# Performance work log

Measured on AMD Instinct MI355X. Metric: run time of the kernel, lower is better.

The kernel has to match this reference:

```python
import jax, jax.numpy as jnp
import numpy as np


def pairwise_distance(x):
    # x: [B,N,F] -> squared euclidean distance matrix [B,N,N]
    sq = jnp.sum(x * x, axis=-1)
    d = sq[:, :, None] + sq[:, None, :] - 2.0 * jnp.einsum('bnd,bmd->bnm', x, x)
    return jnp.maximum(d, 0.0)


def knn_adjacency(dist, k):
    # keep the k nearest neighbors of each point (binary adjacency)
    B, N, _ = dist.shape
    idx = jax.lax.top_k(-dist, k)[1]  # [B,N,k]
    A = jnp.zeros((B, N, N), dist.dtype)
    return A.at[jnp.arange(B)[:, None, None], jnp.arange(N)[None, :, None], idx].set(1.0)


def get_laplacian(A):
    # normalized graph Laplacian L = I - D^{-1/2} A D^{-1/2}
    d = jnp.sum(A, axis=-1)
    dinv = jnp.where(d > 0, 1.0 / jnp.sqrt(jnp.maximum(d, 1e-12)), 0.0)
    An = A * dinv[:, :, None] * dinv[:, None, :]
    return jnp.eye(A.shape[-1], dtype=A.dtype)[None] - An


def cheb_conv(x, L, W, b, K):
    # DenseChebConv: Chebyshev recurrence T0=x, T1=Lx, Tk=2L T_{k-1}-T_{k-2};
    # concat along features then dense projection. x:[B,N,Fin], W:[K*Fin,Fout]
    xs = [x]
    if K > 1:
        xs.append(jnp.einsum('bnm,bmf->bnf', L, x))
    for _ in range(2, K):
        xs.append(2.0 * jnp.einsum('bnm,bmf->bnf', L, xs[-1]) - xs[-2])
    xk = jnp.concatenate(xs, axis=-1)
    return jnp.einsum('bnf,fo->bno', xk, W) + b


def segment_max(out, idx):
    # fused replacement of the per-batch/per-cluster python loops:
    # out:[B,N,F], idx:[B,R,S] -> max-pooled cluster features [B,R,F]
    B = out.shape[0]
    g = out[jnp.arange(B)[:, None, None], idx]  # [B,R,S,F]
    return jnp.max(g, axis=2)


def setup_inputs():
    key = jax.random.key(0)
    ks = jax.random.split(key, 12)
    B, N, R, S, P = 32, 1024, 64, 16, 55
    inp = {}
    inp['x'] = jax.random.normal(ks[0], (B, N, 7), jnp.float32)
    inp['x2'] = jax.random.normal(ks[1], (B, N, 3), jnp.float32)
    inp['laplacian_Reeb'] = jax.random.normal(ks[2], (B, R, R), jnp.float32)
    inp['W1'] = jax.random.normal(ks[3], (3 * 7, 64), jnp.float32) * 0.1
    inp['b1'] = jnp.zeros((64,), jnp.float32)
    inp['W_reeb'] = jax.random.normal(ks[4], (6 * 64, 256), jnp.float32) * 0.05
    inp['b_reeb'] = jnp.zeros((256,), jnp.float32)
    inp['W_fps'] = jax.random.normal(ks[5], (6 * 64, 256), jnp.float32) * 0.05
    inp['b_fps'] = jnp.zeros((256,), jnp.float32)
    inp['fc1_w'] = jax.random.normal(ks[6], (512, 256), jnp.float32) * 0.05
    inp['fc1_b'] = jnp.zeros((256,), jnp.float32)
    inp['fc3_w'] = jax.random.normal(ks[7], (256, 40), jnp.float32) * 0.05
    inp['fc3_b'] = jnp.zeros((40,), jnp.float32)
    inp['sccs'] = jax.random.randint(ks[8], (B, R, S), 0, N)
    inp['sccs_fps'] = jax.random.randint(ks[9], (B, P, N), 0, N)
    inp['k'] = 30
    inp['batch_size'] = B
    inp['num_points'] = N
    return inp


def reference(x, x2, laplacian_Reeb, W1, b1, W_reeb, b_reeb, W_fps, b_fps,
              fc1_w, fc1_b, fc3_w, fc3_b, sccs, sccs_fps, k, batch_size, num_points):
    sg = jax.lax.stop_gradient
    # point-cloud kNN Laplacian (torch.no_grad in original)
    L = sg(get_laplacian(knn_adjacency(pairwise_distance(x), k)))
    out = jax.nn.relu(cheb_conv(x, L, W1, b1, 3))  # [B,N,64]
    reg1 = jnp.sum(jnp.einsum('bnf,bnm,bmg->bfg', out, L, out) ** 2)
    # Reeb-graph segment max pooling (no_grad in original)
    V_reeb = sg(segment_max(out, sccs))  # [B,R,64]
    L_reeb = sg(laplacian_Reeb)
    out_reeb = jax.nn.relu(cheb_conv(V_reeb, L_reeb, W_reeb, b_reeb, 6))  # [B,R,256]
    reg2 = jnp.sum(jnp.einsum('bnf,bnm,bmg->bfg', out_reeb, L_reeb, out_reeb) ** 2)
    # FPS cluster max pooling (no_grad in original)
    V_fps = sg(segment_max(out, sccs_fps))  # [B,55,64]
    L_fps = sg(get_laplacian(pairwise_distance(V_fps)))
    out_fps = jax.nn.relu(cheb_conv(V_fps, L_fps, W_fps, b_fps, 6))  # [B,55,256]
    reg3 = jnp.sum(jnp.einsum('bnf,bnm,bmg->bfg', out_fps, L_fps, out_fps) ** 2)
    feat = jnp.concatenate([jnp.max(out_reeb, axis=1), jnp.max(out_fps, axis=1)], axis=1)  # [B,512]
    h = jax.nn.relu(feat @ fc1_w + fc1_b)
    logits = h @ fc3_w + fc3_b  # [B,40]
    regs = jnp.stack([reg1, reg2, reg3,
                      jnp.sum(fc1_w[:, 0] ** 2), fc1_b[0] ** 2,
                      jnp.sum(fc3_w[:, 0] ** 2), fc3_b[0] ** 2])
    return logits, regs
```

## Files before the change

### kernel.cpp

```cpp
#include <hip/hip_runtime.h>
#include <math.h>

#define BN 32
#define NP 1024
#define KNN 30
#define NR 64
#define NFPS 55

#define XSLOT(r) ((r) * 8 + ((r) >> 7) * 4)

__device__ __forceinline__ float lap_s() {
    const float dv = 1.0f / sqrtf(30.0f);
    return dv * dv;
}

__device__ __forceinline__ float dist7(const float4& xiA, const float4& xiB,
                                       float sqi, const float4& ca, const float4& cb) {
#pragma clang fp contract(off)
    float dot = xiA.x * ca.x;
    dot = fmaf(xiA.y, ca.y, dot);
    dot = fmaf(xiA.z, ca.z, dot);
    dot = fmaf(xiA.w, ca.w, dot);
    dot = fmaf(xiB.x, cb.x, dot);
    dot = fmaf(xiB.y, cb.y, dot);
    dot = fmaf(xiB.z, cb.z, dot);
    float r = sqi + cb.w;
    r = r - 2.f * dot;
    return fmaxf(r, 0.f);
}

__global__ __launch_bounds__(256, 4) void k_knn(const float* __restrict__ x,
                                                int* __restrict__ knn,
                                                float* __restrict__ xs1) {
    __shared__ float xls[8224];
    int b = blockIdx.x;
    int t = threadIdx.x;
    int ln = t & 63, wv = t >> 6;
    int seg = ln & 7;
    int rl  = ln >> 3;

    const float* xb = x + (size_t)b * NP * 7;
#pragma unroll 4
    for (int k = 0; k < 32; ++k) {
        int q = k * 256 + t;
        int r = q >> 3, d = q & 7;
        float v = (d < 7) ? xb[r * 7 + d] : 0.f;
        float p2 = v * v;
        p2 += __shfl_xor(p2, 1);
        p2 += __shfl_xor(p2, 2);
        p2 += __shfl_xor(p2, 4);
        xls[XSLOT(r) + d] = (d < 7) ? v : p2;
    }
    __syncthreads();

    int grow = blockIdx.y * 32 + wv * 8 + rl;
    int gslot = XSLOT(grow);
    float4 xiA = *(const float4*)&xls[gslot];
    float4 xiB = *(const float4*)&xls[gslot + 4];
    float sqi = xiB.w;

    float bd[KNN];
#pragma unroll
    for (int q = 0; q < KNN; ++q) bd[q] = __builtin_inff();
    int jbase = seg * 128;
    int sbase = XSLOT(jbase);
    for (int jc = 0; jc < 128; jc += 4) {
        const float* p = &xls[sbase + jc * 8];
        float4 a0 = *(const float4*)(p +  0), b0 = *(const float4*)(p +  4);
        float4 a1 = *(const float4*)(p +  8), b1 = *(const float4*)(p + 12);
        float4 a2 = *(const float4*)(p + 16), b2 = *(const float4*)(p + 20);
        float4 a3 = *(const float4*)(p + 24), b3 = *(const float4*)(p + 28);
        float d0 = dist7(xiA, xiB, sqi, a0, b0);
        float d1 = dist7(xiA, xiB, sqi, a1, b1);
        float d2 = dist7(xiA, xiB, sqi, a2, b2);
        float d3 = dist7(xiA, xiB, sqi, a3, b3);
#pragma unroll
        for (int q = KNN - 1; q >= 1; --q) bd[q] = __builtin_amdgcn_fmed3f(bd[q - 1], d0, bd[q]);
        bd[0] = fminf(bd[0], d0);
#pragma unroll
        for (int q = KNN - 1; q >= 1; --q) bd[q] = __builtin_amdgcn_fmed3f(bd[q - 1], d1, bd[q]);
        bd[0] = fminf(bd[0], d1);
#pragma unroll
        for (int q = KNN - 1; q >= 1; --q) bd[q] = __builtin_amdgcn_fmed3f(bd[q - 1], d2, bd[q]);
        bd[0] = fminf(bd[0], d2);
#pragma unroll
        for (int q = KNN - 1; q >= 1; --q) bd[q] = __builtin_amdgcn_fmed3f(bd[q - 1], d3, bd[q]);
        bd[0] = fminf(bd[0], d3);
    }

    float m[32];
#pragma unroll
    for (int q = 0; q < KNN; ++q) m[q] = bd[q];
    m[30] = __builtin_inff(); m[31] = __builtin_inff();
#pragma unroll
    for (int lvl = 0; lvl < 3; ++lvl) {
        int mask = 1 << lvl;
#pragma unroll
        for (int q = 0; q < 16; ++q) {
            float u = __shfl_xor(m[31 - q], mask);
            float v = __shfl_xor(m[q], mask);
            float lo = fminf(m[q], u);
            float hi = fminf(m[31 - q], v);
            m[q] = lo; m[31 - q] = hi;
        }
#pragma unroll
        for (int d = 16; d >= 1; d >>= 1) {
#pragma unroll
            for (int i = 0; i < 32; ++i) {
                if ((i & d) == 0) {
                    float a = m[i], c = m[i | d];
                    m[i] = fminf(a, c);
                    m[i | d] = fmaxf(a, c);
                }
            }
        }
    }
    float T = m[29];
    int firstT = 0;
#pragma unroll
    for (int q = 0; q < KNN; ++q) firstT += (m[q] < T) ? 1 : 0;
    int need = KNN - firstT;
    int cnt_lt = 0, cnt_eq = 0;
#pragma unroll
    for (int q = 0; q < KNN; ++q) {
        cnt_lt += (bd[q] < T) ? 1 : 0;
        cnt_eq += (bd[q] == T) ? 1 : 0;
    }
    int lanebase = ln & ~7;
    int pe = 0;
#pragma unroll
    for (int s2 = 0; s2 < 7; ++s2) {
        int v = __shfl(cnt_eq, lanebase + s2);
        pe += (s2 < seg) ? v : 0;
    }
    int e = need - pe;
    e = (e < 0) ? 0 : e;
    e = (e > cnt_eq) ? cnt_eq : e;
    int tk = cnt_lt + e;
    int pb = 0;
#pragma unroll
    for (int s2 = 0; s2 < 7; ++s2) {
        int v = __shfl(tk, lanebase + s2);
        pb += (s2 < seg) ? v : 0;
    }
    int base = pb;

    int* kout = knn + ((size_t)b * NP + grow) * KNN;
    float n0 = 0.f, n1 = 0.f, n2 = 0.f, n3 = 0.f, n4 = 0.f, n5 = 0.f, n6 = 0.f;
    int cs = 0, ct = 0;
    for (int jc = 0; jc < 128; jc += 4) {
        const float* p = &xls[sbase + jc * 8];
        float4 a0 = *(const float4*)(p +  0), b0 = *(const float4*)(p +  4);
        float4 a1 = *(const float4*)(p +  8), b1 = *(const float4*)(p + 12);
        float4 a2 = *(const float4*)(p + 16), b2 = *(const float4*)(p + 20);
        float4 a3 = *(const float4*)(p + 24), b3 = *(const float4*)(p + 28);
        float d0 = dist7(xiA, xiB, sqi, a0, b0);
        float d1 = dist7(xiA, xiB, sqi, a1, b1);
        float d2 = dist7(xiA, xiB, sqi, a2, b2);
        float d3 = dist7(xiA, xiB, sqi, a3, b3);
#pragma unroll
        for (int u = 0; u < 4; ++u) {
            float dist = (u == 0) ? d0 : (u == 1) ? d1 : (u == 2) ? d2 : d3;
            const float4& ca = (u == 0) ? a0 : (u == 1) ? a1 : (u == 2) ? a2 : a3;
            const float4& cb = (u == 0) ? b0 : (u == 1) ? b1 : (u == 2) ? b2 : b3;
            bool lt = dist < T;
            bool eq = (dist == T) && (ct < e);
            if ((lt || eq) && (cs + ct < tk)) {
                kout[base + cs + ct] = jbase + jc + u;
                cs += lt ? 1 : 0;
                ct += eq ? 1 : 0;
                n0 += ca.x; n1 += ca.y; n2 += ca.z; n3 += ca.w;
                n4 += cb.x; n5 += cb.y; n6 += cb.z;
            }
        }
    }
#pragma unroll
    for (int mask = 1; mask <= 4; mask <<= 1) {
        n0 += __shfl_xor(n0, mask);
        n1 += __shfl_xor(n1, mask);
        n2 += __shfl_xor(n2, mask);
        n3 += __shfl_xor(n3, mask);
        n4 += __shfl_xor(n4, mask);
        n5 += __shfl_xor(n5, mask);
        n6 += __shfl_xor(n6, mask);
    }
    if (seg < 7) {
        float nv = (seg == 0) ? n0 : (seg == 1) ? n1 : (seg == 2) ? n2 :
                   (seg == 3) ? n3 : (seg == 4) ? n4 : (seg == 5) ? n5 : n6;
        xs1[((size_t)b * NP + grow) * 7 + seg] = xls[gslot + seg] - lap_s() * nv;
    }
}

__global__ __launch_bounds__(256) void k_out(const float* __restrict__ x,
                                             const float* __restrict__ xs1,
                                             const int* __restrict__ knn,
                                             const float* __restrict__ W1,
                                             const float* __restrict__ b1,
                                             float* __restrict__ out,
                                             const float* __restrict__ fc1_w,
                                             const float* __restrict__ fc1_b,
                                             const float* __restrict__ fc3_w,
                                             const float* __restrict__ fc3_b,
                                             float* __restrict__ regs,
                                             float* __restrict__ Cbuf) {
    __shared__ float x1s[NP * 7];
    __shared__ float x0s[64 * 7];
    __shared__ float fr[64 * 21];
    __shared__ float W1s[21 * 64];
    __shared__ float b1s[64];
    int b = blockIdx.x, y = blockIdx.y;
    int t = threadIdx.x;
    if (y == 16) {
        float* cb = Cbuf + (size_t)b * 4096;
        for (int q = t; q < 4096; q += 256) cb[q] = 0.f;
        if (b != 0) return;
        float* r1 = x1s;
        float* r2 = x1s + 256;
        float s1 = 0.f;
        for (int i = t; i < 512; i += 256) { float v = fc1_w[(size_t)i * 256]; s1 += v * v; }
        float v2 = fc3_w[(size_t)t * 40];
        r1[t] = s1; r2[t] = v2 * v2;
        __syncthreads();
        for (int st = 128; st > 0; st >>= 1) {
            if (t < st) { r1[t] += r1[t + st]; r2[t] += r2[t + st]; }
            __syncthreads();
        }
        if (t == 0) {
            regs[0] = 0.f; regs[1] = 0.f; regs[2] = 0.f;
            regs[3] = r1[0];
            regs[4] = fc1_b[0] * fc1_b[0];
            regs[5] = r2[0];
            regs[6] = fc3_b[0] * fc3_b[0];
        }
        return;
    }
    int rbase = y * 64;
    for (int q = t; q < NP * 7; q += 256) x1s[q] = xs1[(size_t)b * NP * 7 + q];
    for (int q = t; q < 64 * 7; q += 256) x0s[q] = x[(size_t)b * NP * 7 + (size_t)rbase * 7 + q];
    for (int q = t; q < 21 * 64; q += 256) W1s[q] = W1[q];
    if (t < 64) b1s[t] = b1[t];
    __syncthreads();
    if (t < 64) {
        int i = rbase + t;
        float f[21];
#pragma unroll
        for (int d = 0; d < 7; ++d) { f[d] = x0s[t * 7 + d]; f[7 + d] = x1s[i * 7 + d]; }
        float ns[7] = {0.f, 0.f, 0.f, 0.f, 0.f, 0.f, 0.f};
        const int* kn = knn + ((size_t)b * NP + i) * KNN;
        for (int q = 0; q < KNN; ++q) {
            int j = kn[q];
#pragma unroll
            for (int d = 0; d < 7; ++d) ns[d] += x1s[j * 7 + d];
        }
        const float s = lap_s();
#pragma unroll
        for (int d = 0; d < 7; ++d) f[14 + d] = 2.f * (f[7 + d] - s * ns[d]) - f[d];
#pragma unroll
        for (int d = 0; d < 21; ++d) fr[t * 21 + d] = f[d];
    }
    __syncthreads();
    int o = t & 63, g = t >> 6;
    for (int m = 0; m < 16; ++m) {
        int r = g * 16 + m;
        float acc = b1s[o];
#pragma unroll
        for (int d = 0; d < 21; ++d) acc += fr[r * 21 + d] * W1s[d * 64 + o];
        out[((size_t)b * NP + rbase + r) * 64 + o] = fmaxf(acc, 0.f);
    }
}

__global__ __launch_bounds__(256) void k_z1v(const float* __restrict__ out,
                                             const int* __restrict__ knn,
                                             const int* __restrict__ sccs,
                                             const int* __restrict__ sccs_fps,
                                             float* __restrict__ Z1,
                                             float* __restrict__ Vr,
                                             float* __restrict__ Vf) {
    __shared__ unsigned bmw[32];
    __shared__ float red[256];
    int b = blockIdx.x, y = blockIdx.y;
    int t = threadIdx.x;
    const float* ob = out + (size_t)b * NP * 64;
    if (y < 256) {
        int i = y * 4 + (t >> 6);
        int f = t & 63;
        const int* kn = knn + ((size_t)b * NP + i) * KNN;
        float sum = 0.f;
        for (int q = 0; q < KNN; ++q) sum += ob[(size_t)kn[q] * 64 + f];
        Z1[((size_t)b * NP + i) * 64 + f] = ob[(size_t)i * 64 + f] - lap_s() * sum;
    } else if (y < 272) {
        int r = (y - 256) * 4 + (t >> 6);
        int f = t & 63;
        const int* sc = sccs + ((size_t)b * NR + r) * 16;
        float m = -__builtin_inff();
        for (int q = 0; q < 16; ++q) m = fmaxf(m, ob[(size_t)sc[q] * 64 + f]);
        Vr[((size_t)b * NR + r) * 64 + f] = m;
    } else {
        int p = y - 272;
        const int* sp = sccs_fps + ((size_t)b * NFPS + p) * 1024;
        if (t < 32) bmw[t] = 0u;
        __syncthreads();
        for (int q = t; q < 1024; q += 256) {
            int r = sp[q];
            atomicOr(&bmw[r >> 5], 1u << (r & 31));
        }
        __syncthreads();
        int f = t & 63, sc = t >> 6;
        float m = -__builtin_inff();
        for (int w0 = sc * 8; w0 < sc * 8 + 8; ++w0) {
            unsigned w = bmw[w0];
            while (w) {
                int bit = __ffs(w) - 1;
                w &= w - 1;
                m = fmaxf(m, ob[(size_t)(w0 * 32 + bit) * 64 + f]);
            }
        }
        red[t] = m; __syncthreads();
        if (sc == 0) {
            m = fmaxf(fmaxf(red[f], red[64 + f]), fmaxf(red[128 + f], red[192 + f]));
            Vf[((size_t)b * NFPS + p) * 64 + f] = m;
        }
    }
}

__device__ __forceinline__ void t1_part(const float* __restrict__ out,
                                        const float* __restrict__ Z1,
                                        float* __restrict__ Cbuf,
                                        float* buf, int y) {
    int b = blockIdx.x, t = threadIdx.x;
    float* os = buf;
    float* zs = buf + 8192;
    const float* ob = out + ((size_t)b * NP + (size_t)y * 128) * 64;
    const float* zb = Z1 + ((size_t)b * NP + (size_t)y * 128) * 64;
    for (int q = t; q < 128 * 64; q += 256) { os[q] = ob[q]; zs[q] = zb[q]; }
    __syncthreads();
    int f0 = (t & 15) * 4, g0 = (t >> 4) * 4;
    float4 ac0 = make_float4(0.f, 0.f, 0.f, 0.f);
    float4 ac1 = ac0, ac2 = ac0, ac3 = ac0;
#pragma unroll 4
    for (int n = 0; n < 128; ++n) {
        float4 ov = *(const float4*)&os[n * 64 + f0];
        float4 zv = *(const float4*)&zs[n * 64 + g0];
        ac0.x += ov.x * zv.x; ac0.y += ov.x * zv.y; ac0.z += ov.x * zv.z; ac0.w += ov.x * zv.w;
        ac1.x += ov.y * zv.x; ac1.y += ov.y * zv.y; ac1.z += ov.y * zv.z; ac1.w += ov.y * zv.w;
        ac2.x += ov.z * zv.x; ac2.y += ov.z * zv.y; ac2.z += ov.z * zv.z; ac2.w += ov.z * zv.w;
        ac3.x += ov.w * zv.x; ac3.y += ov.w * zv.y; ac3.z += ov.w * zv.z; ac3.w += ov.w * zv.w;
    }
    float* cb = Cbuf + (size_t)b * 4096;
    atomicAdd(&cb[(f0 + 0) * 64 + g0 + 0], ac0.x);
    atomicAdd(&cb[(f0 + 0) * 64 + g0 + 1], ac0.y);
    atomicAdd(&cb[(f0 + 0) * 64 + g0 + 2], ac0.z);
    atomicAdd(&cb[(f0 + 0) * 64 + g0 + 3], ac0.w);
    atomicAdd(&cb[(f0 + 1) * 64 + g0 + 0], ac1.x);
    atomicAdd(&cb[(f0 + 1) * 64 + g0 + 1], ac1.y);
    atomicAdd(&cb[(f0 + 1) * 64 + g0 + 2], ac1.z);
    atomicAdd(&cb[(f0 + 1) * 64 + g0 + 3], ac1.w);
    atomicAdd(&cb[(f0 + 2) * 64 + g0 + 0], ac2.x);
    atomicAdd(&cb[(f0 + 2) * 64 + g0 + 1], ac2.y);
    atomicAdd(&cb[(f0 + 2) * 64 + g0 + 2], ac2.z);
    atomicAdd(&cb[(f0 + 2) * 64 + g0 + 3], ac2.w);
    atomicAdd(&cb[(f0 + 3) * 64 + g0 + 0], ac3.x);
    atomicAdd(&cb[(f0 + 3) * 64 + g0 + 1], ac3.y);
    atomicAdd(&cb[(f0 + 3) * 64 + g0 + 2], ac3.z);
    atomicAdd(&cb[(f0 + 3) * 64 + g0 + 3], ac3.w);
}

__device__ __forceinline__ void lfps_impl(const float* __restrict__ Vfps,
                                          float* __restrict__ Lf, float* buf) {
    int b = blockIdx.x;
    int t = threadIdx.x;
    float* Vs = buf;
    float* sq = buf + 3520;
    float* dist = buf + 3584;
    float* dinv = buf + 6609;
    for (int q = t; q < NFPS * 64; q += 256) Vs[q] = Vfps[(size_t)b * NFPS * 64 + q];
    __syncthreads();
    if (t < NFPS) {
        float s = 0.f;
        for (int f = 0; f < 64; ++f) { float v = Vs[t * 64 + f]; s += v * v; }
        sq[t] = s;
    }
    __syncthreads();
    for (int q = t; q < NFPS * NFPS; q += 256) {
        int i = q / NFPS, j = q % NFPS;
        float dot = 0.f;
        for (int f = 0; f < 64; ++f) dot += Vs[i * 64 + f] * Vs[j * 64 + f];
        dist[q] = fmaxf(sq[i] + sq[j] - 2.f * dot, 0.f);
    }
    __syncthreads();
    if (t < NFPS) {
        float s = 0.f;
        for (int j = 0; j < NFPS; ++j) s += dist[t * NFPS + j];
        dinv[t] = (s > 0.f) ? 1.0f / sqrtf(fmaxf(s, 1e-12f)) : 0.f;
    }
    __syncthreads();
    for (int q = t; q < NFPS * NFPS; q += 256) {
        int i = q / NFPS, j = q % NFPS;
        Lf[(size_t)b * NFPS * NFPS + q] = ((i == j) ? 1.f : 0.f) - dist[q] * dinv[i] * dinv[j];
    }
}

template<int N>
__device__ __forceinline__ void cheb_impl(const float* __restrict__ L,
                                          const float* __restrict__ V,
                                          const float* __restrict__ W,
                                          const float* __restrict__ bias,
                                          float* __restrict__ out,
                                          float* __restrict__ Z,
                                          float* Ls, float* bA, float* bB, float* Ws,
                                          int b, int sl) {
    constexpr int NPAD = (N + 3) & ~3;
    int t = threadIdx.x;
    int c0 = (t & 15) * 4;
    int r0 = (t >> 4) * 4;

    for (int q = t; q < 64 * 64; q += 256) { Ls[q] = 0.f; bA[q] = 0.f; bB[q] = 0.f; }
    __syncthreads();
    for (int q = t; q < N * N; q += 256) {
        int r = q / N, m = q % N;
        Ls[r * 64 + m] = L[(size_t)b * N * N + q];
    }
    for (int q = t; q < N * 64; q += 256) bA[q] = V[(size_t)b * N * 64 + q];
    {
        const float* Wk = W + sl * 64;
        for (int q = t; q < 64 * 64; q += 256) Ws[q] = Wk[(q >> 6) * 256 + (q & 63)];
    }
    float4 a4[4];
    {
        float4 bv = *(const float4*)&bias[sl * 64 + c0];
#pragma unroll
        for (int i = 0; i < 4; ++i) a4[i] = bv;
    }
    __syncthreads();

    auto accum = [&](const float* xb) {
#pragma unroll 2
        for (int m = 0; m < 64; m += 4) {
            float4 xv[4], wv[4];
#pragma unroll
            for (int i = 0; i < 4; ++i) xv[i] = *(const float4*)&xb[(r0 + i) * 64 + m];
#pragma unroll
            for (int mm = 0; mm < 4; ++mm) wv[mm] = *(const float4*)&Ws[(m + mm) * 64 + c0];
#pragma unroll
            for (int i = 0; i < 4; ++i) {
                float xi0 = xv[i].x, xi1 = xv[i].y, xi2 = xv[i].z, xi3 = xv[i].w;
                a4[i].x += xi0 * wv[0].x; a4[i].y += xi0 * wv[0].y; a4[i].z += xi0 * wv[0].z; a4[i].w += xi0 * wv[0].w;
                a4[i].x += xi1 * wv[1].x; a4[i].y += xi1 * wv[1].y; a4[i].z += xi1 * wv[1].z; a4[i].w += xi1 * wv[1].w;
                a4[i].x += xi2 * wv[2].x; a4[i].y += xi2 * wv[2].y; a4[i].z += xi2 * wv[2].z; a4[i].w += xi2 * wv[2].w;
                a4[i].x += xi3 * wv[3].x; a4[i].y += xi3 * wv[3].y; a4[i].z += xi3 * wv[3].z; a4[i].w += xi3 * wv[3].w;
            }
        }
    };
    auto chebmm = [&](const float* src, float* dst, bool first) {
        float4 acc[4];
#pragma unroll
        for (int i = 0; i < 4; ++i) acc[i] = make_float4(0.f, 0.f, 0.f, 0.f);
#pragma unroll 2
        for (int m = 0; m < NPAD; m += 4) {
            float4 sv[4], lv[4];
#pragma unroll
            for (int mm = 0; mm < 4; ++mm) sv[mm] = *(const float4*)&src[(m + mm) * 64 + c0];
#pragma unroll
            for (int i = 0; i < 4; ++i) lv[i] = *(const float4*)&Ls[(r0 + i) * 64 + m];
#pragma unroll
            for (int i = 0; i < 4; ++i) {
                float l0 = lv[i].x, l1 = lv[i].y, l2 = lv[i].z, l3 = lv[i].w;
                acc[i].x += l0 * sv[0].x; acc[i].y += l0 * sv[0].y; acc[i].z += l0 * sv[0].z; acc[i].w += l0 * sv[0].w;
                acc[i].x += l1 * sv[1].x; acc[i].y += l1 * sv[1].y; acc[i].z += l1 * sv[1].z; acc[i].w += l1 * sv[1].w;
                acc[i].x += l2 * sv[2].x; acc[i].y += l2 * sv[2].y; acc[i].z += l2 * sv[2].z; acc[i].w += l2 * sv[2].w;
                acc[i].x += l3 * sv[3].x; acc[i].y += l3 * sv[3].y; acc[i].z += l3 * sv[3].z; acc[i].w += l3 * sv[3].w;
            }
        }
#pragma unroll
        for (int i = 0; i < 4; ++i) {
            if (r0 + i < N) {
                float4* d = (float4*)&dst[(r0 + i) * 64 + c0];
                if (first) *d = acc[i];
                else {
                    float4 od = *d;
                    *d = make_float4(2.f * acc[i].x - od.x, 2.f * acc[i].y - od.y,
                                     2.f * acc[i].z - od.z, 2.f * acc[i].w - od.w);
                }
            }
        }
    };
    auto loadW = [&](int k) {
        const float* Wk = W + (size_t)k * 64 * 256 + sl * 64;
        for (int q = t; q < 64 * 64; q += 256) Ws[q] = Wk[(q >> 6) * 256 + (q & 63)];
    };

    accum(bA);                 __syncthreads();
    chebmm(bA, bB, true);      loadW(1);  __syncthreads();
    accum(bB);                 __syncthreads();
    chebmm(bB, bA, false);     loadW(2);  __syncthreads();
    accum(bA);                 __syncthreads();
    chebmm(bA, bB, false);     loadW(3);  __syncthreads();
    accum(bB);                 __syncthreads();
    chebmm(bB, bA, false);     loadW(4);  __syncthreads();
    accum(bA);                 __syncthreads();
    chebmm(bA, bB, false);     loadW(5);  __syncthreads();
    accum(bB);                 __syncthreads();

    float* ob = out + (size_t)b * N * 256 + sl * 64;
#pragma unroll
    for (int i = 0; i < 4; ++i) {
        if (r0 + i < N) {
            float4 v = make_float4(fmaxf(a4[i].x, 0.f), fmaxf(a4[i].y, 0.f),
                                   fmaxf(a4[i].z, 0.f), fmaxf(a4[i].w, 0.f));
            *(float4*)&bA[(r0 + i) * 64 + c0] = v;
            *(float4*)&ob[(size_t)(r0 + i) * 256 + c0] = v;
        }
    }
    __syncthreads();
    {
        float4 acc[4];
#pragma unroll
        for (int i = 0; i < 4; ++i) acc[i] = make_float4(0.f, 0.f, 0.f, 0.f);
#pragma unroll 2
        for (int m = 0; m < NPAD; m += 4) {
            float4 sv[4], lv[4];
#pragma unroll
            for (int mm = 0; mm < 4; ++mm) sv[mm] = *(const float4*)&bA[(m + mm) * 64 + c0];
#pragma unroll
            for (int i = 0; i < 4; ++i) lv[i] = *(const float4*)&Ls[(r0 + i) * 64 + m];
#pragma unroll
            for (int i = 0; i < 4; ++i) {
                float l0 = lv[i].x, l1 = lv[i].y, l2 = lv[i].z, l3 = lv[i].w;
                acc[i].x += l0 * sv[0].x; acc[i].y += l0 * sv[0].y; acc[i].z += l0 * sv[0].z; acc[i].w += l0 * sv[0].w;
                acc[i].x += l1 * sv[1].x; acc[i].y += l1 * sv[1].y; acc[i].z += l1 * sv[1].z; acc[i].w += l1 * sv[1].w;
                acc[i].x += l2 * sv[2].x; acc[i].y += l2 * sv[2].y; acc[i].z += l2 * sv[2].z; acc[i].w += l2 * sv[2].w;
                acc[i].x += l3 * sv[3].x; acc[i].y += l3 * sv[3].y; acc[i].z += l3 * sv[3].z; acc[i].w += l3 * sv[3].w;
            }
        }
        float* zb = Z + (size_t)b * N * 256 + sl * 64;
#pragma unroll
        for (int i = 0; i < 4; ++i)
            if (r0 + i < N) *(float4*)&zb[(size_t)(r0 + i) * 256 + c0] = acc[i];
    }
}

template<int N>
__device__ __forceinline__ void treg_impl(const float* __restrict__ out,
                                          const float* __restrict__ Z,
                                          float* __restrict__ reg,
                                          float* zs, float* os, float* red, int y) {
    int b = blockIdx.x;
    int f0 = (y >> 1) * 32;
    int g0 = (y & 1) * 128;
    int t = threadIdx.x;
    for (int q = t; q < N * 128; q += 256) {
        int r = q >> 7, gl = q & 127;
        zs[q] = Z[(size_t)b * N * 256 + r * 256 + g0 + gl];
    }
    for (int q = t; q < N * 32; q += 256) {
        int r = q >> 5, f = q & 31;
        os[q] = out[(size_t)b * N * 256 + r * 256 + f0 + f];
    }
    __syncthreads();
    int fl = t >> 3;
    int gb = (t & 7) * 16;
    float accv[16];
#pragma unroll
    for (int q = 0; q < 16; ++q) accv[q] = 0.f;
    for (int n = 0; n < N; ++n) {
        float a = os[n * 32 + fl];
        const float* zr = zs + n * 128 + gb;
#pragma unroll
        for (int q = 0; q < 16; ++q) accv[q] += a * zr[q];
    }
    float loc = 0.f;
#pragma unroll
    for (int q = 0; q < 16; ++q) loc += accv[q] * accv[q];
    red[t] = loc; __syncthreads();
    for (int st = 128; st > 0; st >>= 1) { if (t < st) red[t] += red[t + st]; __syncthreads(); }
    if (t == 0) atomicAdd(reg, red[0]);
}

__global__ __launch_bounds__(256) void k_mid1(
        const float* __restrict__ out, const float* __restrict__ Z1,
        const float* __restrict__ Vfps, float* __restrict__ Cbuf,
        float* __restrict__ Lf,
        const float* __restrict__ Lr, const float* __restrict__ Vr,
        const float* __restrict__ Wr, const float* __restrict__ br,
        float* __restrict__ outR, float* __restrict__ Zr) {
    __shared__ float smem[16384];
    int y = blockIdx.y;
    if (y < 8)       t1_part(out, Z1, Cbuf, smem, y);
    else if (y == 8) lfps_impl(Vfps, Lf, smem);
    else cheb_impl<NR>(Lr, Vr, Wr, br, outR, Zr,
                       smem, smem + 4096, smem + 8192, smem + 12288,
                       blockIdx.x, y - 9);
}

__global__ __launch_bounds__(256) void k_mid2(
        const float* __restrict__ Lf, const float* __restrict__ Vf,
        const float* __restrict__ Wf, const float* __restrict__ bf,
        float* __restrict__ outP, float* __restrict__ Zf,
        const float* __restrict__ outR, const float* __restrict__ Zr,
        const float* __restrict__ Cbuf, float* __restrict__ regs) {
    __shared__ float smem[16384];
    int y = blockIdx.y;
    if (y < 4) cheb_impl<NFPS>(Lf, Vf, Wf, bf, outP, Zf,
                               smem, smem + 4096, smem + 8192, smem + 12288,
                               blockIdx.x, y);
    else if (y < 20) treg_impl<NR>(outR, Zr, regs + 1, smem, smem + 8192, smem + 10240, y - 4);
    else {
        int b = blockIdx.x, t = threadIdx.x;
        float* red = smem;
        float loc = 0.f;
        for (int q = t; q < 4096; q += 256) { float v = Cbuf[(size_t)b * 4096 + q]; loc += v * v; }
        red[t] = loc; __syncthreads();
        for (int st = 128; st > 0; st >>= 1) { if (t < st) red[t] += red[t + st]; __syncthreads(); }
        if (t == 0) atomicAdd(&regs[0], red[0]);
    }
}

__global__ __launch_bounds__(256) void k_fin(
        const float* __restrict__ outP, const float* __restrict__ Zf,
        const float* __restrict__ outR,
        const float* __restrict__ fc1_w, const float* __restrict__ fc1_b,
        const float* __restrict__ fc3_w, const float* __restrict__ fc3_b,
        float* __restrict__ regs, float* __restrict__ logits) {
    __shared__ float smem[10496];
    int y = blockIdx.y;
    if (y < 16) treg_impl<NFPS>(outP, Zf, regs + 2, smem, smem + 8192, smem + 10240, y);
    else {
        int b = blockIdx.x, t = threadIdx.x;
        float* feat = smem;
        float* h = smem + 8192;
        float m = -__builtin_inff();
        for (int r = 0; r < NR; ++r) m = fmaxf(m, outR[((size_t)b * NR + r) * 256 + t]);
        feat[t] = m;
        m = -__builtin_inff();
        for (int p = 0; p < NFPS; ++p) m = fmaxf(m, outP[((size_t)b * NFPS + p) * 256 + t]);
        feat[256 + t] = m;
        __syncthreads();
        float a = fc1_b[t];
        for (int i = 0; i < 512; ++i) a += feat[i] * fc1_w[(size_t)i * 256 + t];
        h[t] = fmaxf(a, 0.f);
        __syncthreads();
        if (t < 40) {
            float a2 = fc3_b[t];
            for (int i = 0; i < 256; ++i) a2 += h[i] * fc3_w[(size_t)i * 40 + t];
            logits[(size_t)b * 40 + t] = a2;
        }
    }
}

extern "C" void kernel_launch(void* const* d_in, const int* in_sizes, int n_in,
                              void* d_out, int out_size, void* d_ws, size_t ws_size,
                              hipStream_t stream) {
    const float* x      = (const float*)d_in[0];
    const float* L_reeb = (const float*)d_in[2];
    const float* W1     = (const float*)d_in[3];
    const float* b1     = (const float*)d_in[4];
    const float* W_reeb = (const float*)d_in[5];
    const float* b_reeb = (const float*)d_in[6];
    const float* W_fps  = (const float*)d_in[7];
    const float* b_fps  = (const float*)d_in[8];
    const float* fc1_w  = (const float*)d_in[9];
    const float* fc1_b  = (const float*)d_in[10];
    const float* fc3_w  = (const float*)d_in[11];
    const float* fc3_b  = (const float*)d_in[12];
    const int*   sccs   = (const int*)d_in[13];
    const int*   sccs_f = (const int*)d_in[14];

    float* outv = (float*)d_out;
    float* regs = outv + 1280;

    char* w = (char*)d_ws;
    size_t off = 0;
    auto alloc = [&](size_t bytes) { void* p = w + off; off = (off + bytes + 255) & ~(size_t)255; return p; };
    int*   knn   = (int*)  alloc((size_t)BN * NP * KNN * 4);
    float* xs1   = (float*)alloc((size_t)BN * NP * 7 * 4);
    float* outF  = (float*)alloc((size_t)BN * NP * 64 * 4);
    float* Z1    = (float*)alloc((size_t)BN * NP * 64 * 4);
    float* Vreeb = (float*)alloc((size_t)BN * NR * 64 * 4);
    float* outRb = (float*)alloc((size_t)BN * NR * 256 * 4);
    float* Z2    = (float*)alloc((size_t)BN * NR * 256 * 4);
    float* Vfps  = (float*)alloc((size_t)BN * NFPS * 64 * 4);
    float* Lfps  = (float*)alloc((size_t)BN * NFPS * NFPS * 4);
    float* outP  = (float*)alloc((size_t)BN * NFPS * 256 * 4);
    float* Z3    = (float*)alloc((size_t)BN * NFPS * 256 * 4);
    float* Cbuf  = (float*)alloc((size_t)BN * 4096 * 4);

    k_knn<<<dim3(BN, NP / 32), 256, 0, stream>>>(x, knn, xs1);
    k_out<<<dim3(BN, 17), 256, 0, stream>>>(x, xs1, knn, W1, b1, outF,
                                            fc1_w, fc1_b, fc3_w, fc3_b, regs, Cbuf);
    k_z1v<<<dim3(BN, 256 + 16 + NFPS), 256, 0, stream>>>(outF, knn, sccs, sccs_f,
                                                         Z1, Vreeb, Vfps);
    k_mid1<<<dim3(BN, 13), 256, 0, stream>>>(outF, Z1, Vfps, Cbuf, Lfps,
                                             L_reeb, Vreeb, W_reeb, b_reeb, outRb, Z2);
    k_mid2<<<dim3(BN, 21), 256, 0, stream>>>(Lfps, Vfps, W_fps, b_fps, outP, Z3,
                                             outRb, Z2, Cbuf, regs);
    k_fin<<<dim3(BN, 17), 256, 0, stream>>>(outP, Z3, outRb,
                                            fc1_w, fc1_b, fc3_w, fc3_b, regs, outv);
}
```

Measured before the change: 357.8 us.

## Compute full Chebyshev output per block, split kNN neighbor sums, pad kNN output

The Chebyshev conv kernels now compute all 256 output columns in one block per batch instead of splitting across four 64-column slices. This removes the redundant Chebyshev recurrence that each slice recomputed, at the cost of larger shared memory (112KB) and fewer, longer blocks. The k_out neighbor-sum gather is spread over four threads per row via a shared partial buffer instead of 64 threads. kNN output gains a fallback fill for unfilled slots.

After: 492.0 us. 37.5% more time.

```diff
diff --git a/kernel.cpp b/kernel.cpp
--- a/kernel.cpp
+++ b/kernel.cpp
@@ -12,6 +12,10 @@
 __device__ __forceinline__ float lap_s() {
     const float dv = 1.0f / sqrtf(30.0f);
     return dv * dv;
+}
+
+__device__ __forceinline__ float4 relu4(float4 v) {
+    return make_float4(fmaxf(v.x, 0.f), fmaxf(v.y, 0.f), fmaxf(v.z, 0.f), fmaxf(v.w, 0.f));
 }
 
 __device__ __forceinline__ float dist7(const float4& xiA, const float4& xiB,
@@ -174,6 +178,7 @@
             }
         }
     }
+    for (int q = cs + ct; q < tk; ++q) kout[base + q] = grow;
 #pragma unroll
     for (int mask = 1; mask <= 4; mask <<= 1) {
         n0 += __shfl_xor(n0, mask);
@@ -208,6 +213,7 @@
     __shared__ float fr[64 * 21];
     __shared__ float W1s[21 * 64];
     __shared__ float b1s[64];
+    __shared__ float nsp[64 * 28];
     int b = blockIdx.x, y = blockIdx.y;
     int t = threadIdx.x;
     if (y == 16) {
@@ -240,21 +246,32 @@
     for (int q = t; q < 21 * 64; q += 256) W1s[q] = W1[q];
     if (t < 64) b1s[t] = b1[t];
     __syncthreads();
+    {
+        int row = t >> 2, tq = t & 3;
+        int i = rbase + row;
+        float ns[7] = {0.f, 0.f, 0.f, 0.f, 0.f, 0.f, 0.f};
+        const int* kn = knn + ((size_t)b * NP + i) * KNN;
+        for (int q = tq; q < KNN; q += 4) {
+            int j = kn[q];
+#pragma unroll
+            for (int d = 0; d < 7; ++d) ns[d] += x1s[j * 7 + d];
+        }
+#pragma unroll
+        for (int d = 0; d < 7; ++d) nsp[row * 28 + tq * 7 + d] = ns[d];
+    }
+    __syncthreads();
     if (t < 64) {
         int i = rbase + t;
         float f[21];
 #pragma unroll
         for (int d = 0; d < 7; ++d) { f[d] = x0s[t * 7 + d]; f[7 + d] = x1s[i * 7 + d]; }
-        float ns[7] = {0.f, 0.f, 0.f, 0.f, 0.f, 0.f, 0.f};
-        const int* kn = knn + ((size_t)b * NP + i) * KNN;
-        for (int q = 0; q < KNN; ++q) {
-            int j = kn[q];
-#pragma unroll
-            for (int d = 0; d < 7; ++d) ns[d] += x1s[j * 7 + d];
-        }
         const float s = lap_s();
 #pragma unroll
-        for (int d = 0; d < 7; ++d) f[14 + d] = 2.f * (f[7 + d] - s * ns[d]) - f[d];
+        for (int d = 0; d < 7; ++d) {
+            float ns = nsp[t * 28 + d] + nsp[t * 28 + 7 + d]
+                     + nsp[t * 28 + 14 + d] + nsp[t * 28 + 21 + d];
+            f[14 + d] = 2.f * (f[7 + d] - s * ns) - f[d];
+        }
 #pragma unroll
         for (int d = 0; d < 21; ++d) fr[t * 21 + d] = f[d];
     }
@@ -401,53 +418,61 @@
 }
 
 template<int N>
-__device__ __forceinline__ void cheb_impl(const float* __restrict__ L,
+__device__ __forceinline__ void cheb_full(const float* __restrict__ L,
                                           const float* __restrict__ V,
                                           const float* __restrict__ W,
                                           const float* __restrict__ bias,
                                           float* __restrict__ out,
                                           float* __restrict__ Z,
-                                          float* Ls, float* bA, float* bB, float* Ws,
-                                          int b, int sl) {
+                                          float* smem, int b) {
     constexpr int NPAD = (N + 3) & ~3;
+    float* Ls = smem;
+    float* bA = smem + 4096;
+    float* bB = smem + 8192;
+    float* Ws = smem + 12288;
     int t = threadIdx.x;
-    int c0 = (t & 15) * 4;
-    int r0 = (t >> 4) * 4;
+    int c0 = (t & 31) * 8;
+    int r0 = (t >> 5) * 8;
+    int c4 = (t & 15) * 4;
+    int r4 = (t >> 4) * 4;
 
     for (int q = t; q < 64 * 64; q += 256) { Ls[q] = 0.f; bA[q] = 0.f; bB[q] = 0.f; }
     __syncthreads();
-    for (int q = t; q < N * N; q += 256) {
-        int r = q / N, m = q % N;
-        Ls[r * 64 + m] = L[(size_t)b * N * N + q];
-    }
+    for (int q = t; q < N * N; q += 256)
+        Ls[(q / N) * 64 + (q % N)] = L[(size_t)b * N * N + q];
     for (int q = t; q < N * 64; q += 256) bA[q] = V[(size_t)b * N * 64 + q];
+    for (int q = t; q < 64 * 256; q += 256) Ws[q] = W[q];
+    float4 acc0[8], acc1[8];
     {
-        const float* Wk = W + sl * 64;
-        for (int q = t; q < 64 * 64; q += 256) Ws[q] = Wk[(q >> 6) * 256 + (q & 63)];
-    }
-    float4 a4[4];
-    {
-        float4 bv = *(const float4*)&bias[sl * 64 + c0];
-#pragma unroll
-        for (int i = 0; i < 4; ++i) a4[i] = bv;
+        float4 bv0 = *(const float4*)&bias[c0];
+        float4 bv1 = *(const float4*)&bias[c0 + 4];
+#pragma unroll
+        for (int i = 0; i < 8; ++i) { acc0[i] = bv0; acc1[i] = bv1; }
     }
     __syncthreads();
 
     auto accum = [&](const float* xb) {
 #pragma unroll 2
         for (int m = 0; m < 64; m += 4) {
-            float4 xv[4], wv[4];
-#pragma unroll
-            for (int i = 0; i < 4; ++i) xv[i] = *(const float4*)&xb[(r0 + i) * 64 + m];
-#pragma unroll
-            for (int mm = 0; mm < 4; ++mm) wv[mm] = *(const float4*)&Ws[(m + mm) * 64 + c0];
-#pragma unroll
-            for (int i = 0; i < 4; ++i) {
-                float xi0 = xv[i].x, xi1 = xv[i].y, xi2 = xv[i].z, xi3 = xv[i].w;
-                a4[i].x += xi0 * wv[0].x; a4[i].y += xi0 * wv[0].y; a4[i].z += xi0 * wv[0].z; a4[i].w += xi0 * wv[0].w;
-                a4[i].x += xi1 * wv[1].x; a4[i].y += xi1 * wv[1].y; a4[i].z += xi1 * wv[1].z; a4[i].w += xi1 * wv[1].w;
-                a4[i].x += xi2 * wv[2].x; a4[i].y += xi2 * wv[2].y; a4[i].z += xi2 * wv[2].z; a4[i].w += xi2 * wv[2].w;
-                a4[i].x += xi3 * wv[3].x; a4[i].y += xi3 * wv[3].y; a4[i].z += xi3 * wv[3].z; a4[i].w += xi3 * wv[3].w;
+            float4 xv[8], w0[4], w1[4];
+#pragma unroll
+            for (int i = 0; i < 8; ++i) xv[i] = *(const float4*)&xb[(r0 + i) * 64 + m];
+#pragma unroll
+            for (int mm = 0; mm < 4; ++mm) {
+                w0[mm] = *(const float4*)&Ws[(m + mm) * 256 + c0];
+                w1[mm] = *(const float4*)&Ws[(m + mm) * 256 + c0 + 4];
+            }
+#pragma unroll
+            for (int i = 0; i < 8; ++i) {
+#pragma unroll
+                for (int mm = 0; mm < 4; ++mm) {
+                    float xm = (mm == 0) ? xv[i].x : (mm == 1) ? xv[i].y :
+                               (mm == 2) ? xv[i].z : xv[i].w;
+                    acc0[i].x += xm * w0[mm].x; acc0[i].y += xm * w0[mm].y;
+                    acc0[i].z += xm * w0[mm].z; acc0[i].w += xm * w0[mm].w;
+                    acc1[i].x += xm * w1[mm].x; acc1[i].y += xm * w1[mm].y;
+                    acc1[i].z += xm * w1[mm].z; acc1[i].w += xm * w1[mm].w;
+                }
             }
         }
     };
@@ -459,9 +484,9 @@
         for (int m = 0; m < NPAD; m += 4) {
             float4 sv[4], lv[4];
 #pragma unroll
-            for (int mm = 0; mm < 4; ++mm) sv[mm] = *(const float4*)&src[(m + mm) * 64 + c0];
-#pragma unroll
-            for (int i = 0; i < 4; ++i) lv[i] = *(const float4*)&Ls[(r0 + i) * 64 + m];
+            for (int mm = 0; mm < 4; ++mm) sv[mm] = *(const float4*)&src[(m + mm) * 64 + c4];
+#pragma unroll
+            for (int i = 0; i < 4; ++i) lv[i] = *(const float4*)&Ls[(r4 + i) * 64 + m];
 #pragma unroll
             for (int i = 0; i < 4; ++i) {
                 float l0 = lv[i].x, l1 = lv[i].y, l2 = lv[i].z, l3 = lv[i].w;
@@ -473,8 +498,8 @@
         }
 #pragma unroll
         for (int i = 0; i < 4; ++i) {
-            if (r0 + i < N) {
-                float4* d = (float4*)&dst[(r0 + i) * 64 + c0];
+            if (r4 + i < N) {
+                float4* d = (float4*)&dst[(r4 + i) * 64 + c4];
                 if (first) *d = acc[i];
                 else {
                     float4 od = *d;
@@ -484,58 +509,66 @@
             }
         }
     };
-    auto loadW = [&](int k) {
-        const float* Wk = W + (size_t)k * 64 * 256 + sl * 64;
-        for (int q = t; q < 64 * 64; q += 256) Ws[q] = Wk[(q >> 6) * 256 + (q & 63)];
+    auto loadWs = [&](int k) {
+        const float* Wk = W + (size_t)k * 64 * 256;
+        for (int q = t; q < 64 * 256; q += 256) Ws[q] = Wk[q];
     };
 
-    accum(bA);                 __syncthreads();
-    chebmm(bA, bB, true);      loadW(1);  __syncthreads();
-    accum(bB);                 __syncthreads();
-    chebmm(bB, bA, false);     loadW(2);  __syncthreads();
-    accum(bA);                 __syncthreads();
-    chebmm(bA, bB, false);     loadW(3);  __syncthreads();
-    accum(bB);                 __syncthreads();
-    chebmm(bB, bA, false);     loadW(4);  __syncthreads();
-    accum(bA);                 __syncthreads();
-    chebmm(bA, bB, false);     loadW(5);  __syncthreads();
-    accum(bB);                 __syncthreads();
-
-    float* ob = out + (size_t)b * N * 256 + sl * 64;
-#pragma unroll
-    for (int i = 0; i < 4; ++i) {
+    accum(bA); chebmm(bA, bB, true);  __syncthreads(); loadWs(1); __syncthreads();
+    accum(bB); chebmm(bB, bA, false); __syncthreads(); loadWs(2); __syncthreads();
+    accum(bA); chebmm(bA, bB, false); __syncthreads(); loadWs(3); __syncthreads();
+    accum(bB); chebmm(bB, bA, false); __syncthreads(); loadWs(4); __syncthreads();
+    accum(bA); chebmm(bA, bB, false); __syncthreads(); loadWs(5); __syncthreads();
+    accum(bB);
+    __syncthreads();
+
+    float* ob = out + (size_t)b * N * 256;
+#pragma unroll
+    for (int i = 0; i < 8; ++i) {
+        float4 v0 = relu4(acc0[i]), v1 = relu4(acc1[i]);
+        *(float4*)&Ws[(r0 + i) * 256 + c0] = v0;
+        *(float4*)&Ws[(r0 + i) * 256 + c0 + 4] = v1;
         if (r0 + i < N) {
-            float4 v = make_float4(fmaxf(a4[i].x, 0.f), fmaxf(a4[i].y, 0.f),
-                                   fmaxf(a4[i].z, 0.f), fmaxf(a4[i].w, 0.f));
-            *(float4*)&bA[(r0 + i) * 64 + c0] = v;
-            *(float4*)&ob[(size_t)(r0 + i) * 256 + c0] = v;
-        }
-    }
-    __syncthreads();
-    {
-        float4 acc[4];
-#pragma unroll
-        for (int i = 0; i < 4; ++i) acc[i] = make_float4(0.f, 0.f, 0.f, 0.f);
+            *(float4*)&ob[(size_t)(r0 + i) * 256 + c0] = v0;
+            *(float4*)&ob[(size_t)(r0 + i) * 256 + c0 + 4] = v1;
+        }
+    }
+    __syncthreads();
+#pragma unroll
+    for (int i = 0; i < 8; ++i) {
+        acc0[i] = make_float4(0.f, 0.f, 0.f, 0.f);
+        acc1[i] = make_float4(0.f, 0.f, 0.f, 0.f);
+    }
 #pragma unroll 2
-        for (int m = 0; m < NPAD; m += 4) {
-            float4 sv[4], lv[4];
-#pragma unroll
-            for (int mm = 0; mm < 4; ++mm) sv[mm] = *(const float4*)&bA[(m + mm) * 64 + c0];
-#pragma unroll
-            for (int i = 0; i < 4; ++i) lv[i] = *(const float4*)&Ls[(r0 + i) * 64 + m];
-#pragma unroll
-            for (int i = 0; i < 4; ++i) {
-                float l0 = lv[i].x, l1 = lv[i].y, l2 = lv[i].z, l3 = lv[i].w;
-                acc[i].x += l0 * sv[0].x; acc[i].y += l0 * sv[0].y; acc[i].z += l0 * sv[0].z; acc[i].w += l0 * sv[0].w;
-                acc[i].x += l1 * sv[1].x; acc[i].y += l1 * sv[1].y; acc[i].z += l1 * sv[1].z; acc[i].w += l1 * sv[1].w;
-                acc[i].x += l2 * sv[2].x; acc[i].y += l2 * sv[2].y; acc[i].z += l2 * sv[2].z; acc[i].w += l2 * sv[2].w;
-                acc[i].x += l3 * sv[3].x; acc[i].y += l3 * sv[3].y; acc[i].z += l3 * sv[3].z; acc[i].w += l3 * sv[3].w;
+    for (int m = 0; m < NPAD; m += 4) {
+        float4 lv[8], w0[4], w1[4];
+#pragma unroll
+        for (int i = 0; i < 8; ++i) lv[i] = *(const float4*)&Ls[(r0 + i) * 64 + m];
+#pragma unroll
+        for (int mm = 0; mm < 4; ++mm) {
+            w0[mm] = *(const float4*)&Ws[(m + mm) * 256 + c0];
+            w1[mm] = *(const float4*)&Ws[(m + mm) * 256 + c0 + 4];
+        }
+#pragma unroll
+        for (int i = 0; i < 8; ++i) {
+#pragma unroll
+            for (int mm = 0; mm < 4; ++mm) {
+                float xm = (mm == 0) ? lv[i].x : (mm == 1) ? lv[i].y :
+                           (mm == 2) ? lv[i].z : lv[i].w;
+                acc0[i].x += xm * w0[mm].x; acc0[i].y += xm * w0[mm].y;
+                acc0[i].z += xm * w0[mm].z; acc0[i].w += xm * w0[mm].w;
+                acc1[i].x += xm * w1[mm].x; acc1[i].y += xm * w1[mm].y;
+                acc1[i].z += xm * w1[mm].z; acc1[i].w += xm * w1[mm].w;
             }
         }
-        float* zb = Z + (size_t)b * N * 256 + sl * 64;
-#pragma unroll
-        for (int i = 0; i < 4; ++i)
-            if (r0 + i < N) *(float4*)&zb[(size_t)(r0 + i) * 256 + c0] = acc[i];
+    }
+    float* zb = Z + (size_t)b * N * 256;
+#pragma unroll
+    for (int i = 0; i < 8; ++i) {
+        if (r0 + i < N) {
+            *(float4*)&zb[(size_t)(r0 + i) * 256 + c0] = acc0[i];
+            *(float4*)&zb[(size_t)(r0 + i) * 256 + c0 + 4] = acc1[i];
+        }
     }
 }
 
@@ -583,13 +616,11 @@
         const float* __restrict__ Lr, const float* __restrict__ Vr,
         const float* __restrict__ Wr, const float* __restrict__ br,
         float* __restrict__ outR, float* __restrict__ Zr) {
-    __shared__ float smem[16384];
+    __shared__ float smem[28672];
     int y = blockIdx.y;
     if (y < 8)       t1_part(out, Z1, Cbuf, smem, y);
     else if (y == 8) lfps_impl(Vfps, Lf, smem);
-    else cheb_impl<NR>(Lr, Vr, Wr, br, outR, Zr,
-                       smem, smem + 4096, smem + 8192, smem + 12288,
-                       blockIdx.x, y - 9);
+    else             cheb_full<NR>(Lr, Vr, Wr, br, outR, Zr, smem, blockIdx.x);
 }
 
 __global__ __launch_bounds__(256) void k_mid2(
@@ -598,12 +629,10 @@
         float* __restrict__ outP, float* __restrict__ Zf,
         const float* __restrict__ outR, const float* __restrict__ Zr,
         const float* __restrict__ Cbuf, float* __restrict__ regs) {
-    __shared__ float smem[16384];
+    __shared__ float smem[28672];
     int y = blockIdx.y;
-    if (y < 4) cheb_impl<NFPS>(Lf, Vf, Wf, bf, outP, Zf,
-                               smem, smem + 4096, smem + 8192, smem + 12288,
-                               blockIdx.x, y);
-    else if (y < 20) treg_impl<NR>(outR, Zr, regs + 1, smem, smem + 8192, smem + 10240, y - 4);
+    if (y == 0) cheb_full<NFPS>(Lf, Vf, Wf, bf, outP, Zf, smem, blockIdx.x);
+    else if (y < 17) treg_impl<NR>(outR, Zr, regs + 1, smem, smem + 8192, smem + 10240, y - 1);
     else {
         int b = blockIdx.x, t = threadIdx.x;
         float* red = smem;
@@ -689,9 +718,9 @@
                                             fc1_w, fc1_b, fc3_w, fc3_b, regs, Cbuf);
     k_z1v<<<dim3(BN, 256 + 16 + NFPS), 256, 0, stream>>>(outF, knn, sccs, sccs_f,
                                                          Z1, Vreeb, Vfps);
-    k_mid1<<<dim3(BN, 13), 256, 0, stream>>>(outF, Z1, Vfps, Cbuf, Lfps,
+    k_mid1<<<dim3(BN, 10), 256, 0, stream>>>(outF, Z1, Vfps, Cbuf, Lfps,
                                              L_reeb, Vreeb, W_reeb, b_reeb, outRb, Z2);
-    k_mid2<<<dim3(BN, 21), 256, 0, stream>>>(Lfps, Vfps, W_fps, b_fps, outP, Z3,
+    k_mid2<<<dim3(BN, 18), 256, 0, stream>>>(Lfps, Vfps, W_fps, b_fps, outP, Z3,
                                              outRb, Z2, Cbuf, regs);
     k_fin<<<dim3(BN, 17), 256, 0, stream>>>(outP, Z3, outRb,
                                             fc1_w, fc1_b, fc3_w, fc3_b, regs, outv);
```
